# Kernel tuning notes

Hardware: AMD Instinct MI355X
Metric: run time of the kernel (lower is better)

## Reference

```python
import jax, jax.numpy as jnp
import numpy as np

# Dimensions (from init_kwargs)
B, Q, C = 2, 40000, 128      # batch, BEV queries (200x200), d_model
NH, NP = 8, 4                 # n_heads, n_points per head
H, W = 90, 160                # value feature-map spatial shape (len = H*W)
HD = C // NH                  # head dim


def setup_inputs() -> dict:
    key = jax.random.key(0)
    ks = jax.random.split(key, 8)
    s = 0.02
    return {
        "query": jax.random.normal(ks[0], (B, Q, C), jnp.float32),
        "value": jax.random.normal(ks[1], (B, H * W, C), jnp.float32),
        "ref_points": jax.random.uniform(ks[2], (B, Q, 2), jnp.float32),  # normalized [0,1] (x, y)
        "W_value": jax.random.normal(ks[3], (C, C), jnp.float32) * s,
        "b_value": jnp.zeros((C,), jnp.float32),
        "W_offset": jax.random.normal(ks[4], (C, NH * NP * 2), jnp.float32) * s,
        "b_offset": jnp.zeros((NH * NP * 2,), jnp.float32),
        "W_attn": jax.random.normal(ks[5], (C, NH * NP), jnp.float32) * s,
        "b_attn": jnp.zeros((NH * NP,), jnp.float32),
        "W_out": jax.random.normal(ks[6], (C, C), jnp.float32) * s,
        "b_out": jnp.zeros((C,), jnp.float32),
    }


def _bilinear_sample(value, loc):
    """value: [B, H*W, NH, HD]; loc: [B, Q, NH, NP, 2] normalized in [0,1].
    Bilinear grid-sample with zero padding outside (align_corners=False).
    Returns [B, Q, NH, NP, HD]."""
    x = loc[..., 0] * W - 0.5
    y = loc[..., 1] * H - 0.5
    x0 = jnp.floor(x)
    y0 = jnp.floor(y)
    wx = x - x0
    wy = y - y0
    x0i = x0.astype(jnp.int32)
    y0i = y0.astype(jnp.int32)
    v = jnp.transpose(value, (0, 2, 1, 3))  # [B, NH, HW, HD] for per-head gather

    def corner(xi, yi, w):
        valid = ((xi >= 0) & (xi < W) & (yi >= 0) & (yi < H)).astype(value.dtype)
        idx = jnp.clip(yi, 0, H - 1) * W + jnp.clip(xi, 0, W - 1)  # [B, Q, NH, NP]
        i = jnp.transpose(idx, (0, 2, 1, 3))                        # [B, NH, Q, NP]
        g = jax.vmap(jax.vmap(lambda vb, ib: vb[ib]))(v, i)         # [B, NH, Q, NP, HD]
        g = jnp.transpose(g, (0, 2, 1, 3, 4))                       # [B, Q, NH, NP, HD]
        return g * (w * valid)[..., None]

    return (corner(x0i, y0i, (1.0 - wx) * (1.0 - wy))
            + corner(x0i + 1, y0i, wx * (1.0 - wy))
            + corner(x0i, y0i + 1, (1.0 - wx) * wy)
            + corner(x0i + 1, y0i + 1, wx * wy))


def reference(query, value, ref_points, W_value, b_value, W_offset, b_offset,
              W_attn, b_attn, W_out, b_out):
    # value projection, split into heads
    v = (value @ W_value + b_value).reshape(B, H * W, NH, HD)
    # per-query learned sampling offsets (in pixels) and attention weights
    offsets = (query @ W_offset + b_offset).reshape(B, Q, NH, NP, 2)
    attn = jax.nn.softmax((query @ W_attn + b_attn).reshape(B, Q, NH, NP), axis=-1)
    # sampling locations, normalized
    norm = jnp.array([W, H], jnp.float32)
    loc = ref_points[:, :, None, None, :] + offsets / norm  # [B, Q, NH, NP, 2]
    sampled = _bilinear_sample(v, loc)                       # [B, Q, NH, NP, HD]
    agg = jnp.einsum('bqhpd,bqhp->bqhd', sampled, attn).reshape(B, Q, C)
    return agg @ W_out + b_out
```

## Files before the change

### kernel.cpp

```cpp
#include <hip/hip_runtime.h>
#include <hip/hip_bf16.h>

#define BB 2
#define QQ 40000
#define CC 128
#define NHH 8
#define NPP 4
#define HH 90
#define WW 160
#define HWW (HH*WW)
#define BQ (BB*QQ)
#define BHW (BB*HWW)

typedef __attribute__((ext_vector_type(8))) short short8;
typedef __attribute__((ext_vector_type(4))) float f32x4;

static __device__ inline short f2bf(float f) {
    __hip_bfloat16 h = __float2bfloat16(f);
    return __builtin_bit_cast(short, h);
}

__global__ __launch_bounds__(256) void prep_weights(
    const float* __restrict__ Wv, const float* __restrict__ Wo,
    const float* __restrict__ Wa, const float* __restrict__ Wout,
    const float* __restrict__ bo, const float* __restrict__ ba,
    short* __restrict__ wtv, short* __restrict__ wcat,
    short* __restrict__ woutt, float* __restrict__ bcat)
{
    const int t = blockIdx.x * 256 + threadIdx.x;
    const int stride = gridDim.x * 256;
    for (int i = t; i < 128 * 128; i += stride) {
        int n = i >> 7, k = i & 127;
        wtv[i] = f2bf(Wv[k * 128 + n]);
    }
    for (int i = t; i < 96 * 128; i += stride) {
        int n = i >> 7, k = i & 127;
        float w = (n < 64) ? Wo[k * 64 + n] : Wa[k * 32 + (n - 64)];
        wcat[i] = f2bf(w);
    }
    for (int i = t; i < 128 * 128; i += stride) {
        int n = i >> 7, k = i & 127;
        woutt[i] = f2bf(Wout[k * 128 + n]);
    }
    if (t < 96) bcat[t] = (t < 64) ? bo[t] : ba[t - 64];
}

template<int N, bool OUT_BF16>
__global__ __launch_bounds__(256) void mfma_gemm_k128(
    const float* __restrict__ X, const short* __restrict__ Wt,
    const float* __restrict__ bias, void* __restrict__ Yv)
{
    constexpr int CT = N / 32;
    __shared__ short sX[128 * 128];
    __shared__ short sW[N * 128];
    const int tid = threadIdx.x;
    const long r0 = (long)blockIdx.x * 128;

    for (int i = tid; i < 128 * 32; i += 256) {
        int rr = i >> 5;
        int c4 = (i & 31) * 4;
        float4 xv = reinterpret_cast<const float4*>(X + (r0 + rr) * 128)[i & 31];
        int byo = (rr * 256 + c4 * 2) ^ ((rr & 7) << 4);
        short* p = (short*)((char*)sX + byo);
        p[0] = f2bf(xv.x); p[1] = f2bf(xv.y); p[2] = f2bf(xv.z); p[3] = f2bf(xv.w);
    }
    for (int i = tid; i < N * 16; i += 256) {
        int nn = i >> 4;
        int c8 = (i & 15) * 8;
        short8 wv = reinterpret_cast<const short8*>(Wt)[i];
        int byo = (nn * 256 + c8 * 2) ^ ((nn & 7) << 4);
        *(short8*)((char*)sW + byo) = wv;
    }
    __syncthreads();

    const int lane = tid & 63, wid = tid >> 6;
    const int wr = wid >> 1, wc = wid & 1;
    const int l15 = lane & 15, lg = lane >> 4;

    f32x4 acc[4][CT] = {};
    #pragma unroll
    for (int ks = 0; ks < 4; ++ks) {
        short8 a[4], b[CT];
        #pragma unroll
        for (int rt = 0; rt < 4; ++rt) {
            int row = wr * 64 + rt * 16 + l15;
            int byo = (row * 256 + ks * 64 + lg * 16) ^ ((row & 7) << 4);
            a[rt] = *(const short8*)((const char*)sX + byo);
        }
        #pragma unroll
        for (int ct = 0; ct < CT; ++ct) {
            int n = wc * (N / 2) + ct * 16 + l15;
            int byo = (n * 256 + ks * 64 + lg * 16) ^ ((n & 7) << 4);
            b[ct] = *(const short8*)((const char*)sW + byo);
        }
        #pragma unroll
        for (int rt = 0; rt < 4; ++rt)
            #pragma unroll
            for (int ct = 0; ct < CT; ++ct)
                acc[rt][ct] = __builtin_amdgcn_mfma_f32_16x16x32_bf16(
                    a[rt], b[ct], acc[rt][ct], 0, 0, 0);
    }

    #pragma unroll
    for (int rt = 0; rt < 4; ++rt) {
        #pragma unroll
        for (int ct = 0; ct < CT; ++ct) {
            int col = wc * (N / 2) + ct * 16 + l15;
            float bv = bias[col];
            #pragma unroll
            for (int r = 0; r < 4; ++r) {
                long row = r0 + wr * 64 + rt * 16 + lg * 4 + r;
                float val = acc[rt][ct][r] + bv;
                if (OUT_BF16)
                    ((short*)Yv)[row * N + col] = f2bf(val);
                else
                    ((float*)Yv)[row * N + col] = val;
            }
        }
    }
}

__global__ __launch_bounds__(256) void deform_sample(
    const short* __restrict__ v,
    const float* __restrict__ qp,
    const float* __restrict__ ref,
    float* __restrict__ agg)
{
    const int bq   = blockIdx.x * 4 + (threadIdx.x >> 6);
    const int lane = threadIdx.x & 63;
    const int h  = lane >> 3;
    const int dp = lane & 7;
    const int bsel = (bq >= QQ) ? 1 : 0;

    const float rx = ref[(long)bq * 2 + 0] * (float)WW - 0.5f;
    const float ry = ref[(long)bq * 2 + 1] * (float)HH - 0.5f;

    const float* al = qp + (long)bq * 96 + 64 + h * 4;
    float l0 = al[0], l1 = al[1], l2 = al[2], l3 = al[3];
    float m = fmaxf(fmaxf(l0, l1), fmaxf(l2, l3));
    float e0 = __expf(l0 - m), e1 = __expf(l1 - m);
    float e2 = __expf(l2 - m), e3 = __expf(l3 - m);
    float inv = 1.0f / (e0 + e1 + e2 + e3);
    float aw[4] = { e0 * inv, e1 * inv, e2 * inv, e3 * inv };

    const float* ob = qp + (long)bq * 96 + h * 8;
    const short* vb = v + (long)bsel * HWW * 128 + h * 16 + dp * 2;

    float acc0 = 0.0f, acc1 = 0.0f;
    #pragma unroll
    for (int p = 0; p < NPP; ++p) {
        float x = rx + ob[p * 2 + 0];
        float y = ry + ob[p * 2 + 1];
        float x0f = floorf(x), y0f = floorf(y);
        float wx = x - x0f, wy = y - y0f;
        int ix0 = (int)x0f, iy0 = (int)y0f;
        float a = aw[p];
        #pragma unroll
        for (int cy = 0; cy < 2; ++cy) {
            int iy = iy0 + cy;
            float wyc = cy ? wy : (1.0f - wy);
            bool vy = ((unsigned)iy < (unsigned)HH);
            int iyc = min(max(iy, 0), HH - 1);
            #pragma unroll
            for (int cx = 0; cx < 2; ++cx) {
                int ix = ix0 + cx;
                float wxc = cx ? wx : (1.0f - wx);
                bool vx = ((unsigned)ix < (unsigned)WW);
                int ixc = min(max(ix, 0), WW - 1);
                float wgt = (vx && vy) ? (a * wxc * wyc) : 0.0f;
                unsigned u = *reinterpret_cast<const unsigned*>(
                    vb + ((long)iyc * WW + ixc) * 128);
                float g0 = __builtin_bit_cast(float, u << 16);
                float g1 = __builtin_bit_cast(float, u & 0xffff0000u);
                acc0 += wgt * g0;
                acc1 += wgt * g1;
            }
        }
    }
    float2* out2 = reinterpret_cast<float2*>(agg + (long)bq * 128);
    out2[lane] = make_float2(acc0, acc1);
}

extern "C" void kernel_launch(void* const* d_in, const int* in_sizes, int n_in,
                              void* d_out, int out_size, void* d_ws, size_t ws_size,
                              hipStream_t stream) {
    const float* query = (const float*)d_in[0];
    const float* value = (const float*)d_in[1];
    const float* ref   = (const float*)d_in[2];
    const float* Wv    = (const float*)d_in[3];
    const float* bv    = (const float*)d_in[4];
    const float* Wo    = (const float*)d_in[5];
    const float* bo    = (const float*)d_in[6];
    const float* Wa    = (const float*)d_in[7];
    const float* ba    = (const float*)d_in[8];
    const float* Wout  = (const float*)d_in[9];
    const float* bout  = (const float*)d_in[10];
    float* out = (float*)d_out;

    char* ws = (char*)d_ws;
    short* vbf   = (short*)ws;
    ws += (long)BHW * 128 * 2;
    short* wtv   = (short*)ws;  ws += 128 * 128 * 2;
    short* wcat  = (short*)ws;  ws += 96 * 128 * 2;
    short* woutt = (short*)ws;  ws += 128 * 128 * 2;
    float* bcat  = (float*)ws;  ws += 128 * 4;
    float* qp    = (float*)ws;  ws += (long)BQ * 96 * 4;
    float* agg   = (float*)ws;

    prep_weights<<<64, 256, 0, stream>>>(Wv, Wo, Wa, Wout, bo, ba,
                                         wtv, wcat, woutt, bcat);
    mfma_gemm_k128<128, true><<<BHW / 128, 256, 0, stream>>>(value, wtv, bv, vbf);
    mfma_gemm_k128<96, false><<<BQ / 128, 256, 0, stream>>>(query, wcat, bcat, qp);
    deform_sample<<<BQ / 4, 256, 0, stream>>>(vbf, qp, ref, agg);
    mfma_gemm_k128<128, false><<<BQ / 128, 256, 0, stream>>>(agg, woutt, bout, out);
}
```

Before: 185.3 us.

## Make GEMMs persistent with register prefetch and store aggregated samples as bf16

The three GEMMs become persistent kernels with a grid capped at 512 blocks. Each block loads its weight tile into shared memory once and prefetches the next X tile into registers while computing the current one, which amortizes weight loads and overlaps global loads with MFMA work. The deform_sample output is now packed to bf16, halving the agg write and the matching read by the output GEMM. This adds register pressure from up to 16 float4 prefetch registers and costs some precision in the intermediate.

```diff
diff --git a/kernel.cpp b/kernel.cpp
--- a/kernel.cpp
+++ b/kernel.cpp
@@ -45,76 +45,118 @@
     if (t < 96) bcat[t] = (t < 64) ? bo[t] : ba[t - 64];
 }
 
-template<int N, bool OUT_BF16>
-__global__ __launch_bounds__(256) void mfma_gemm_k128(
-    const float* __restrict__ X, const short* __restrict__ Wt,
-    const float* __restrict__ bias, void* __restrict__ Yv)
+template<int N, bool XF32, bool OUT_BF16>
+__global__ __launch_bounds__(256, 2) void gemm_pipe(
+    const void* __restrict__ Xv, const short* __restrict__ Wt,
+    const float* __restrict__ bias, void* __restrict__ Yv, int ntiles)
 {
     constexpr int CT = N / 32;
+    __shared__ short sW[N * 128];
     __shared__ short sX[128 * 128];
-    __shared__ short sW[N * 128];
     const int tid = threadIdx.x;
-    const long r0 = (long)blockIdx.x * 128;
-
-    for (int i = tid; i < 128 * 32; i += 256) {
-        int rr = i >> 5;
-        int c4 = (i & 31) * 4;
-        float4 xv = reinterpret_cast<const float4*>(X + (r0 + rr) * 128)[i & 31];
-        int byo = (rr * 256 + c4 * 2) ^ ((rr & 7) << 4);
-        short* p = (short*)((char*)sX + byo);
-        p[0] = f2bf(xv.x); p[1] = f2bf(xv.y); p[2] = f2bf(xv.z); p[3] = f2bf(xv.w);
-    }
+
     for (int i = tid; i < N * 16; i += 256) {
-        int nn = i >> 4;
-        int c8 = (i & 15) * 8;
+        int nn = i >> 4, c8 = (i & 15) * 8;
         short8 wv = reinterpret_cast<const short8*>(Wt)[i];
-        int byo = (nn * 256 + c8 * 2) ^ ((nn & 7) << 4);
-        *(short8*)((char*)sW + byo) = wv;
-    }
-    __syncthreads();
+        *(short8*)((char*)sW + ((nn * 256 + c8 * 2) ^ ((nn & 7) << 4))) = wv;
+    }
 
     const int lane = tid & 63, wid = tid >> 6;
     const int wr = wid >> 1, wc = wid & 1;
     const int l15 = lane & 15, lg = lane >> 4;
 
-    f32x4 acc[4][CT] = {};
+    float bvc[CT];
     #pragma unroll
-    for (int ks = 0; ks < 4; ++ks) {
-        short8 a[4], b[CT];
+    for (int ct = 0; ct < CT; ++ct) bvc[ct] = bias[wc * (N / 2) + ct * 16 + l15];
+
+    float4 xf[16];
+    short8 xb[8];
+
+    int tile = blockIdx.x;
+    if (tile < ntiles) {
+        if (XF32) {
+            const float4* src = reinterpret_cast<const float4*>((const float*)Xv) + (long)tile * 4096;
+            #pragma unroll
+            for (int j = 0; j < 16; ++j) xf[j] = src[j * 256 + tid];
+        } else {
+            const short8* src = reinterpret_cast<const short8*>((const short*)Xv) + (long)tile * 2048;
+            #pragma unroll
+            for (int j = 0; j < 8; ++j) xb[j] = src[j * 256 + tid];
+        }
+    }
+
+    for (; tile < ntiles; tile += gridDim.x) {
+        __syncthreads();
+        if (XF32) {
+            #pragma unroll
+            for (int j = 0; j < 16; ++j) {
+                int flat = j * 256 + tid;
+                int row = flat >> 5, c4 = flat & 31;
+                int byo = (row * 256 + c4 * 8) ^ ((row & 7) << 4);
+                short* p = (short*)((char*)sX + byo);
+                p[0] = f2bf(xf[j].x); p[1] = f2bf(xf[j].y);
+                p[2] = f2bf(xf[j].z); p[3] = f2bf(xf[j].w);
+            }
+        } else {
+            #pragma unroll
+            for (int j = 0; j < 8; ++j) {
+                int flat = j * 256 + tid;
+                int row = flat >> 4, c8 = flat & 15;
+                int byo = (row * 256 + c8 * 16) ^ ((row & 7) << 4);
+                *(short8*)((char*)sX + byo) = xb[j];
+            }
+        }
+        int nt = tile + gridDim.x;
+        if (nt < ntiles) {
+            if (XF32) {
+                const float4* src = reinterpret_cast<const float4*>((const float*)Xv) + (long)nt * 4096;
+                #pragma unroll
+                for (int j = 0; j < 16; ++j) xf[j] = src[j * 256 + tid];
+            } else {
+                const short8* src = reinterpret_cast<const short8*>((const short*)Xv) + (long)nt * 2048;
+                #pragma unroll
+                for (int j = 0; j < 8; ++j) xb[j] = src[j * 256 + tid];
+            }
+        }
+        __syncthreads();
+
+        f32x4 acc[4][CT] = {};
+        #pragma unroll
+        for (int ks = 0; ks < 4; ++ks) {
+            short8 a[4], b[CT];
+            #pragma unroll
+            for (int rt = 0; rt < 4; ++rt) {
+                int row = wr * 64 + rt * 16 + l15;
+                a[rt] = *(const short8*)((const char*)sX +
+                        ((row * 256 + ks * 64 + lg * 16) ^ ((row & 7) << 4)));
+            }
+            #pragma unroll
+            for (int ct = 0; ct < CT; ++ct) {
+                int n = wc * (N / 2) + ct * 16 + l15;
+                b[ct] = *(const short8*)((const char*)sW +
+                        ((n * 256 + ks * 64 + lg * 16) ^ ((n & 7) << 4)));
+            }
+            #pragma unroll
+            for (int rt = 0; rt < 4; ++rt)
+                #pragma unroll
+                for (int ct = 0; ct < CT; ++ct)
+                    acc[rt][ct] = __builtin_amdgcn_mfma_f32_16x16x32_bf16(
+                        a[rt], b[ct], acc[rt][ct], 0, 0, 0);
+        }
+
+        const long r0 = (long)tile * 128;
         #pragma unroll
         for (int rt = 0; rt < 4; ++rt) {
-            int row = wr * 64 + rt * 16 + l15;
-            int byo = (row * 256 + ks * 64 + lg * 16) ^ ((row & 7) << 4);
-            a[rt] = *(const short8*)((const char*)sX + byo);
-        }
-        #pragma unroll
-        for (int ct = 0; ct < CT; ++ct) {
-            int n = wc * (N / 2) + ct * 16 + l15;
-            int byo = (n * 256 + ks * 64 + lg * 16) ^ ((n & 7) << 4);
-            b[ct] = *(const short8*)((const char*)sW + byo);
-        }
-        #pragma unroll
-        for (int rt = 0; rt < 4; ++rt)
-            #pragma unroll
-            for (int ct = 0; ct < CT; ++ct)
-                acc[rt][ct] = __builtin_amdgcn_mfma_f32_16x16x32_bf16(
-                    a[rt], b[ct], acc[rt][ct], 0, 0, 0);
-    }
-
-    #pragma unroll
-    for (int rt = 0; rt < 4; ++rt) {
-        #pragma unroll
-        for (int ct = 0; ct < CT; ++ct) {
-            int col = wc * (N / 2) + ct * 16 + l15;
-            float bv = bias[col];
-            #pragma unroll
-            for (int r = 0; r < 4; ++r) {
-                long row = r0 + wr * 64 + rt * 16 + lg * 4 + r;
-                float val = acc[rt][ct][r] + bv;
-                if (OUT_BF16)
-                    ((short*)Yv)[row * N + col] = f2bf(val);
-                else
-                    ((float*)Yv)[row * N + col] = val;
+            #pragma unroll
+            for (int ct = 0; ct < CT; ++ct) {
+                int col = wc * (N / 2) + ct * 16 + l15;
+                #pragma unroll
+                for (int r = 0; r < 4; ++r) {
+                    long row = r0 + wr * 64 + rt * 16 + lg * 4 + r;
+                    float val = acc[rt][ct][r] + bvc[ct];
+                    if (OUT_BF16) ((short*)Yv)[row * N + col] = f2bf(val);
+                    else          ((float*)Yv)[row * N + col] = val;
+                }
             }
         }
     }
@@ -124,7 +166,7 @@
     const short* __restrict__ v,
     const float* __restrict__ qp,
     const float* __restrict__ ref,
-    float* __restrict__ agg)
+    unsigned* __restrict__ agg)
 {
     const int bq   = blockIdx.x * 4 + (threadIdx.x >> 6);
     const int lane = threadIdx.x & 63;
@@ -177,8 +219,9 @@
             }
         }
     }
-    float2* out2 = reinterpret_cast<float2*>(agg + (long)bq * 128);
-    out2[lane] = make_float2(acc0, acc1);
+    unsigned pk = (unsigned)(unsigned short)f2bf(acc0)
+                | ((unsigned)(unsigned short)f2bf(acc1) << 16);
+    agg[(long)bq * 64 + lane] = pk;
 }
 
 extern "C" void kernel_launch(void* const* d_in, const int* in_sizes, int n_in,
@@ -198,19 +241,23 @@
     float* out = (float*)d_out;
 
     char* ws = (char*)d_ws;
-    short* vbf   = (short*)ws;
-    ws += (long)BHW * 128 * 2;
+    short* vbf   = (short*)ws;  ws += (long)BHW * 128 * 2;
     short* wtv   = (short*)ws;  ws += 128 * 128 * 2;
     short* wcat  = (short*)ws;  ws += 96 * 128 * 2;
     short* woutt = (short*)ws;  ws += 128 * 128 * 2;
     float* bcat  = (float*)ws;  ws += 128 * 4;
     float* qp    = (float*)ws;  ws += (long)BQ * 96 * 4;
-    float* agg   = (float*)ws;
+    unsigned* aggb = (unsigned*)ws;
+
+    const int ntV = BHW / 128;
+    const int ntQ = BQ / 128;
+    const int gV = ntV < 512 ? ntV : 512;
+    const int gQ = ntQ < 512 ? ntQ : 512;
 
     prep_weights<<<64, 256, 0, stream>>>(Wv, Wo, Wa, Wout, bo, ba,
                                          wtv, wcat, woutt, bcat);
-    mfma_gemm_k128<128, true><<<BHW / 128, 256, 0, stream>>>(value, wtv, bv, vbf);
-    mfma_gemm_k128<96, false><<<BQ / 128, 256, 0, stream>>>(query, wcat, bcat, qp);
-    deform_sample<<<BQ / 4, 256, 0, stream>>>(vbf, qp, ref, agg);
-    mfma_gemm_k128<128, false><<<BQ / 128, 256, 0, stream>>>(agg, woutt, bout, out);
-}
+    gemm_pipe<128, true, true><<<gV, 256, 0, stream>>>(value, wtv, bv, vbf, ntV);
+    gemm_pipe<96, true, false><<<gQ, 256, 0, stream>>>(query, wcat, bcat, qp, ntQ);
+    deform_sample<<<BQ / 4, 256, 0, stream>>>(vbf, qp, ref, aggb);
+    gemm_pipe<128, false, false><<<gQ, 256, 0, stream>>>(aggb, woutt, bout, out, ntQ);
+}
```

After: 170.5 us. 1.09x faster.
